# Kernel tuning notes

Measured on AMD Instinct MI355X. Metric: run time of the kernel, lower is better.

## Reference

```python
import jax, jax.numpy as jnp
import numpy as np
from jax import lax

B, S, D, NH, K = 4, 2048, 1024, 16, 3
EPS = 1e-6


def custom_layernorm(x, gamma, beta):
    # torch-style: std with ddof=1, eps added to std (not var)
    mean = jnp.mean(x, axis=-1, keepdims=True)
    var = jnp.sum((x - mean) ** 2, axis=-1, keepdims=True) / (x.shape[-1] - 1)
    std = jnp.sqrt(var)
    return gamma * ((x - mean) / (std + EPS)) + beta


def setup_inputs() -> dict:
    key = jax.random.key(0)
    ks = jax.random.split(key, 10)
    s = 1.0 / np.sqrt(D)
    return {
        "x": jax.random.normal(ks[0], (B, S, D), jnp.float32),
        "Wq": jax.random.normal(ks[1], (D, D), jnp.float32) * s,
        "bq": jax.random.normal(ks[2], (D,), jnp.float32) * 0.02,
        "Wk": jax.random.normal(ks[3], (D, D), jnp.float32) * s,
        "Wv": jax.random.normal(ks[4], (D, D), jnp.float32) * s,
        "bv": jax.random.normal(ks[5], (D,), jnp.float32) * 0.02,
        "conv_w": jax.random.normal(ks[6], (D, D // NH, K), jnp.float32) * (1.0 / np.sqrt((D // NH) * K)),
        "conv_b": jax.random.normal(ks[7], (D,), jnp.float32) * 0.02,
        "gamma": jnp.ones((D,), jnp.float32),
        "beta": jnp.zeros((D,), jnp.float32),
        "Wo": jax.random.normal(ks[8], (D, D), jnp.float32) * s,
        "bo": jax.random.normal(ks[9], (D,), jnp.float32) * 0.02,
    }


def reference(x, Wq, bq, Wk, Wv, bv, conv_w, conv_b, gamma, beta, Wo, bo):
    d = x.shape[-1]
    groups = d // conv_w.shape[1]
    pad = conv_w.shape[2] // 2

    q = x @ Wq + bq
    k = x @ Wk  # key has no bias
    v = x @ Wv + bv

    # grouped conv1d over sequence dim (NCW layout)
    xc = jnp.transpose(x, (0, 2, 1))  # [B, D, S]
    conv_out = lax.conv_general_dilated(
        xc, conv_w, window_strides=(1,), padding=[(pad, pad)],
        feature_group_count=groups,
        dimension_numbers=("NCH", "OIH", "NCH"),
    ) + conv_b[None, :, None]
    conv_out = jnp.transpose(conv_out, (0, 2, 1))  # [B, S, D]
    conv_out = custom_layernorm(conv_out, gamma, beta)  # dropout = identity (eval)

    scale = 1.0 / jnp.sqrt(jnp.asarray(d, x.dtype))
    scores = jnp.einsum("bqd,bkd->bqk", q, k) * scale  # [B, S, S]
    attn = jax.nn.softmax(scores, axis=-1)
    attention_out = jnp.einsum("bqk,bkd->bqd", attn, v)

    combined = custom_layernorm(conv_out + attention_out, gamma, beta)
    return combined @ Wo + bo + x
```

## Files before the change

### kernel.cpp

```cpp
#include <hip/hip_runtime.h>
#include <cstdint>


#define DEV __device__ __forceinline__

typedef unsigned short u16;
typedef __attribute__((ext_vector_type(8))) short bf16x8;
typedef __attribute__((ext_vector_type(4))) float f32x4;

static const int Sn = 2048, Dn = 1024;

DEV float bf2f(u16 u) { union { unsigned int i; float f; } w; w.i = ((unsigned int)u) << 16; return w.f; }
DEV u16 f2bf(float f) {
  union { float f; unsigned int i; } w; w.f = f;
  unsigned int x = w.i;
  return (u16)((x + 0x7FFFu + ((x >> 16) & 1u)) >> 16);
}

DEV void gload_lds16(const u16* gsrc, u16* lds_dst) {
  __builtin_amdgcn_global_load_lds(
      (const __attribute__((address_space(1))) void*)gsrc,
      (__attribute__((address_space(3))) void*)lds_dst,
      16, 0, 0);
}

DEV float block_allreduce_sum(float v, float* red, int tid) {
  #pragma unroll
  for (int o = 32; o > 0; o >>= 1) v += __shfl_down(v, o, 64);
  __syncthreads();
  if ((tid & 63) == 0) red[tid >> 6] = v;
  __syncthreads();
  return red[0] + red[1] + red[2] + red[3];
}

DEV float block_allreduce_max(float v, float* red, int tid) {
  #pragma unroll
  for (int o = 32; o > 0; o >>= 1) v = fmaxf(v, __shfl_down(v, o, 64));
  __syncthreads();
  if ((tid & 63) == 0) red[tid >> 6] = v;
  __syncthreads();
  return fmaxf(fmaxf(red[0], red[1]), fmaxf(red[2], red[3]));
}

__global__ __launch_bounds__(256)
void prep_all(const float* __restrict__ Wq, const float* __restrict__ Wk,
              const float* __restrict__ Wv, const float* __restrict__ Wo,
              u16* __restrict__ wT,
              const float* __restrict__ bq, const float* __restrict__ bv,
              float* __restrict__ qkvb, float* __restrict__ rowsum,
              const float* __restrict__ x, u16* __restrict__ xb) {
  __shared__ u16 sm[64][68];
  int blk = blockIdx.x;
  int tid = threadIdx.x;
  if (blk < 1024) {
    int w = blk >> 8, t = blk & 255;
    const float* src = (w == 0) ? Wq : (w == 1) ? Wk : (w == 2) ? Wv : Wo;
    u16* dst = wT + (size_t)w * 1048576u;
    int i0 = (t >> 4) << 6, j0 = (t & 15) << 6;
    int tx = tid & 15, r0 = tid >> 4;
    #pragma unroll
    for (int rr = r0; rr < 64; rr += 16) {
      float4 v = *(const float4*)&src[(long)(i0 + rr) * 1024 + j0 + tx * 4];
      sm[rr][tx*4+0] = f2bf(v.x); sm[rr][tx*4+1] = f2bf(v.y);
      sm[rr][tx*4+2] = f2bf(v.z); sm[rr][tx*4+3] = f2bf(v.w);
    }
    __syncthreads();
    #pragma unroll
    for (int cc = r0; cc < 64; cc += 16) {
      ushort4 o;
      o.x = sm[tx*4+0][cc]; o.y = sm[tx*4+1][cc];
      o.z = sm[tx*4+2][cc]; o.w = sm[tx*4+3][cc];
      *(ushort4*)&dst[(long)(j0 + cc) * 1024 + i0 + tx * 4] = o;
    }
  } else if (blk == 1024) {
    for (int j = tid; j < 3072; j += 256) {
      float v = 0.0f;
      if (j < 1024) v = bq[j];
      else if (j >= 2048) v = bv[j - 2048];
      qkvb[j] = v;
    }
    for (int j = tid; j < 8192; j += 256) rowsum[j] = 0.0f;
  } else {
    int i = (blk - 1025) * 1024 + tid * 4;
    float4 v = *(const float4*)&x[i];
    ushort4 o;
    o.x = f2bf(v.x); o.y = f2bf(v.y); o.z = f2bf(v.z); o.w = f2bf(v.w);
    *(ushort4*)&xb[i] = o;
  }
}

template<typename CT>
__global__ __launch_bounds__(256, 2)
void gemm_nt(const u16* __restrict__ A, const u16* __restrict__ A2, long Abs, int lda,
             const u16* __restrict__ B, long Bbs, int ldb,
             CT* __restrict__ C, CT* __restrict__ C2, long Cbs, int ldc,
             int zsplit, int K, float scale,
             const float* __restrict__ bias, int bias_bs,
             const float* __restrict__ res, long Rbs, int ldr,
             u16* __restrict__ vtout) {
  __shared__ u16 sA[2][128 * 32];
  __shared__ u16 sB[2][128 * 32];
  int tid = threadIdx.x;
  int lane = tid & 63, wv = tid >> 6;
  int quad = lane >> 4, lm = lane & 15;
  int wr = wv >> 1, wc = wv & 1;
  long m0 = (long)blockIdx.x * 128, n0 = (long)blockIdx.y * 128;
  int z = blockIdx.z;
  if (z >= zsplit) { A = A2 + (long)(z - zsplit) * Abs; C = C2 + (long)(z - zsplit) * Cbs; }
  else             { A = A  + (long)z * Abs;            C = C  + (long)z * Cbs; }
  B += (long)z * Bbs;
  if (res) res += (long)z * Rbs;

  f32x4 acc[4][4] = {};

  int srow = wv * 16 + (lane >> 2);
  int sch = (lane & 3) * 8;
  const u16* Ap = A + (m0 + srow) * (long)lda + sch;
  const u16* Bp = B + (n0 + srow) * (long)ldb + sch;
  const int lofs = wv * 16 * 32;

  for (int k0 = 0; k0 < K; k0 += 64) {
    #pragma unroll
    for (int h = 0; h < 2; h++) {
      int kh = k0 + h * 32;
      gload_lds16(Ap + kh, &sA[h][lofs]);
      gload_lds16(Ap + 64 * (long)lda + kh, &sA[h][lofs + 64 * 32]);
      gload_lds16(Bp + kh, &sB[h][lofs]);
      gload_lds16(Bp + 64 * (long)ldb + kh, &sB[h][lofs + 64 * 32]);
    }
    __syncthreads();
    #pragma unroll
    for (int h = 0; h < 2; h++) {
      bf16x8 af[4], bfr[4];
      #pragma unroll
      for (int mi = 0; mi < 4; mi++)
        af[mi] = *(const bf16x8*)&sA[h][(wr * 64 + mi * 16 + lm) * 32 + quad * 8];
      #pragma unroll
      for (int ni = 0; ni < 4; ni++)
        bfr[ni] = *(const bf16x8*)&sB[h][(wc * 64 + ni * 16 + lm) * 32 + quad * 8];
      #pragma unroll
      for (int mi = 0; mi < 4; mi++)
        #pragma unroll
        for (int ni = 0; ni < 4; ni++)
          acc[mi][ni] = __builtin_amdgcn_mfma_f32_16x16x32_bf16(af[mi], bfr[ni], acc[mi][ni], 0, 0, 0);
    }
    __syncthreads();
  }

  if (sizeof(CT) == 2 && vtout && z == 2) {
    int b = (int)(m0 >> 11);
    long s0 = (m0 & 2047) + wr * 64 + quad * 4;
    #pragma unroll
    for (int ni = 0; ni < 4; ni++) {
      int col = (int)n0 + wc * 64 + ni * 16 + lm;
      float bv = bias ? bias[(long)z * bias_bs + col] : 0.0f;
      u16* vrow = vtout + ((long)b * 1024 + col) * 2048;
      #pragma unroll
      for (int mi = 0; mi < 4; mi++) {
        ushort4 o;
        o.x = f2bf(acc[mi][ni][0] * scale + bv);
        o.y = f2bf(acc[mi][ni][1] * scale + bv);
        o.z = f2bf(acc[mi][ni][2] * scale + bv);
        o.w = f2bf(acc[mi][ni][3] * scale + bv);
        *(ushort4*)&vrow[s0 + mi * 16] = o;
      }
    }
  } else {
    #pragma unroll
    for (int mi = 0; mi < 4; mi++) {
      #pragma unroll
      for (int ni = 0; ni < 4; ni++) {
        int col = (int)n0 + wc * 64 + ni * 16 + lm;
        float bv = bias ? bias[(long)z * bias_bs + col] : 0.0f;
        #pragma unroll
        for (int r = 0; r < 4; r++) {
          long rowg = m0 + wr * 64 + mi * 16 + quad * 4 + r;
          float v = acc[mi][ni][r] * scale + bv;
          if (res) v += res[rowg * (long)ldr + col];
          if constexpr (sizeof(CT) == 2) C[rowg * (long)ldc + col] = f2bf(v);
          else                           C[rowg * (long)ldc + col] = v;
        }
      }
    }
  }
}

__global__ __launch_bounds__(256, 2)
void post_qkv(int ngemm,
              const u16* __restrict__ Qb, const u16* __restrict__ Kb,
              u16* __restrict__ Pd, u16* __restrict__ Pw,
              const u16* __restrict__ Vb, u16* __restrict__ vt,
              float* __restrict__ rowsum) {
  __shared__ u16 smem[2 * 2 * 128 * 32];
  int blk = blockIdx.x;
  int tid = threadIdx.x;
  if (blk < ngemm) {
    u16* sA0 = smem;
    u16* sB0 = smem + 2 * 128 * 32;
    int lane = tid & 63, wv = tid >> 6;
    int quad = lane >> 4, lm = lane & 15;
    int wr = wv >> 1, wc = wv & 1;
    int z = blk >> 8;
    long m0 = (long)(blk & 15) * 128, n0 = (long)((blk >> 4) & 15) * 128;
    const u16* A = Qb + (long)z * Sn * Dn;
    const u16* B = Kb + (long)z * Sn * Dn;
    u16* C = (z < 2) ? Pd + (long)z * Sn * Sn : Pw + (long)(z - 2) * Sn * Sn;

    f32x4 acc[4][4] = {};
    int srow = wv * 16 + (lane >> 2);
    int sch = (lane & 3) * 8;
    const u16* Ap = A + (m0 + srow) * 1024 + sch;
    const u16* Bp = B + (n0 + srow) * 1024 + sch;
    const int lofs = wv * 16 * 32;

    for (int k0 = 0; k0 < 1024; k0 += 64) {
      #pragma unroll
      for (int h = 0; h < 2; h++) {
        int kh = k0 + h * 32;
        gload_lds16(Ap + kh, &sA0[h * 128 * 32 + lofs]);
        gload_lds16(Ap + 64 * 1024 + kh, &sA0[h * 128 * 32 + lofs + 64 * 32]);
        gload_lds16(Bp + kh, &sB0[h * 128 * 32 + lofs]);
        gload_lds16(Bp + 64 * 1024 + kh, &sB0[h * 128 * 32 + lofs + 64 * 32]);
      }
      __syncthreads();
      #pragma unroll
      for (int h = 0; h < 2; h++) {
        bf16x8 af[4], bfr[4];
        #pragma unroll
        for (int mi = 0; mi < 4; mi++)
          af[mi] = *(const bf16x8*)&sA0[h * 128 * 32 + (wr * 64 + mi * 16 + lm) * 32 + quad * 8];
        #pragma unroll
        for (int ni = 0; ni < 4; ni++)
          bfr[ni] = *(const bf16x8*)&sB0[h * 128 * 32 + (wc * 64 + ni * 16 + lm) * 32 + quad * 8];
        #pragma unroll
        for (int mi = 0; mi < 4; mi++)
          #pragma unroll
          for (int ni = 0; ni < 4; ni++)
            acc[mi][ni] = __builtin_amdgcn_mfma_f32_16x16x32_bf16(af[mi], bfr[ni], acc[mi][ni], 0, 0, 0);
      }
      __syncthreads();
    }
    float psum[4][4];
    #pragma unroll
    for (int mi = 0; mi < 4; mi++)
      #pragma unroll
      for (int r = 0; r < 4; r++) psum[mi][r] = 0.0f;
    #pragma unroll
    for (int mi = 0; mi < 4; mi++) {
      #pragma unroll
      for (int ni = 0; ni < 4; ni++) {
        int col = (int)n0 + wc * 64 + ni * 16 + lm;
        #pragma unroll
        for (int r = 0; r < 4; r++) {
          long rowg = m0 + wr * 64 + mi * 16 + quad * 4 + r;
          float e = __expf(acc[mi][ni][r] * 0.03125f);
          psum[mi][r] += e;
          C[rowg * 2048 + col] = f2bf(e);
        }
      }
    }
    #pragma unroll
    for (int mi = 0; mi < 4; mi++)
      #pragma unroll
      for (int r = 0; r < 4; r++) {
        float v = psum[mi][r];
        v += __shfl_xor(v, 1, 64);
        v += __shfl_xor(v, 2, 64);
        v += __shfl_xor(v, 4, 64);
        v += __shfl_xor(v, 8, 64);
        psum[mi][r] = v;
      }
    if (lm == 0) {
      #pragma unroll
      for (int mi = 0; mi < 4; mi++)
        #pragma unroll
        for (int r = 0; r < 4; r++) {
          long rowg = m0 + wr * 64 + mi * 16 + quad * 4 + r;
          unsafeAtomicAdd(&rowsum[(long)z * 2048 + rowg], psum[mi][r]);
        }
    }
  } else {
    u16 (*sm)[68] = (u16(*)[68])smem;
    int t = blk - ngemm;
    int b = t >> 9, r = t & 511;
    int j0 = (r & 15) << 6, i0 = ((r >> 4) & 31) << 6;
    const u16* s = Vb + (long)b * Sn * Dn;
    u16* d = vt + (long)b * Dn * Sn;
    int tx = tid & 15, r0 = tid >> 4;
    #pragma unroll
    for (int rr = r0; rr < 64; rr += 16) {
      ushort4 v = *(const ushort4*)&s[(long)(i0 + rr) * 1024 + j0 + tx * 4];
      sm[rr][tx*4+0] = v.x; sm[rr][tx*4+1] = v.y; sm[rr][tx*4+2] = v.z; sm[rr][tx*4+3] = v.w;
    }
    __syncthreads();
    #pragma unroll
    for (int cc = r0; cc < 64; cc += 16) {
      ushort4 o;
      o.x = sm[tx*4+0][cc]; o.y = sm[tx*4+1][cc];
      o.z = sm[tx*4+2][cc]; o.w = sm[tx*4+3][cc];
      *(ushort4*)&d[(long)(j0 + cc) * 2048 + i0 + tx * 4] = o;
    }
  }
}

__global__ __launch_bounds__(256)
void smax_conv(u16* __restrict__ pa, u16* __restrict__ pb, int rowsplit, int nsm,
               const float* __restrict__ x, const float* __restrict__ cw,
               const float* __restrict__ cb, u16* __restrict__ convo) {
  __shared__ u16 smem[22160];
  __shared__ float red[4];
  int blk = blockIdx.x;
  int tid = threadIdx.x;
  if (blk < nsm) {
    long row = blk;
    u16* p = (row < rowsplit) ? pa + row * 2048 : pb + (row - rowsplit) * 2048;
    ushort4 a = *(const ushort4*)&p[tid * 8];
    ushort4 b = *(const ushort4*)&p[tid * 8 + 4];
    float f0 = bf2f(a.x), f1 = bf2f(a.y), f2 = bf2f(a.z), f3 = bf2f(a.w);
    float f4 = bf2f(b.x), f5 = bf2f(b.y), f6 = bf2f(b.z), f7 = bf2f(b.w);
    float m = fmaxf(fmaxf(fmaxf(f0, f1), fmaxf(f2, f3)),
                    fmaxf(fmaxf(f4, f5), fmaxf(f6, f7)));
    m = block_allreduce_max(m, red, tid);
    float e0 = __expf(f0 - m), e1 = __expf(f1 - m), e2 = __expf(f2 - m), e3 = __expf(f3 - m);
    float e4 = __expf(f4 - m), e5 = __expf(f5 - m), e6 = __expf(f6 - m), e7 = __expf(f7 - m);
    float s = block_allreduce_sum(e0 + e1 + e2 + e3 + e4 + e5 + e6 + e7, red, tid);
    float inv = 1.0f / s;
    ushort4 o1, o2;
    o1.x = f2bf(e0 * inv); o1.y = f2bf(e1 * inv); o1.z = f2bf(e2 * inv); o1.w = f2bf(e3 * inv);
    o2.x = f2bf(e4 * inv); o2.y = f2bf(e5 * inv); o2.z = f2bf(e6 * inv); o2.w = f2bf(e7 * inv);
    *(ushort4*)&p[tid * 8] = o1;
    *(ushort4*)&p[tid * 8 + 4] = o2;
  } else {
    u16 (*sx)[72] = (u16(*)[72])smem;
    u16 (*sw)[200] = (u16(*)[200])(smem + 9360);
    int r = blk - nsm;
    int s0 = (r & 15) * 128;
    int g = (r >> 4) & 15;
    int b = r >> 8;
    int lane = tid & 63, wv = tid >> 6;
    int quad = lane >> 4, lm = lane & 15;
    for (int idx = tid; idx < 64 * 192; idx += 256) {
      int oc = idx / 192, k = idx - oc * 192;
      int t2 = k >> 6, i = k & 63;
      sw[oc][k] = f2bf(cw[((long)(g * 64 + oc)) * 192 + i * 3 + t2]);
    }
    for (int idx = tid; idx < 130 * 16; idx += 256) {
      int rr = idx >> 4, c4 = (idx & 15) * 4;
      int s = s0 - 1 + rr;
      ushort4 v;
      if (s >= 0 && s < Sn) {
        float4 f = *(const float4*)&x[((long)b * Sn + s) * Dn + g * 64 + c4];
        v.x = f2bf(f.x); v.y = f2bf(f.y); v.z = f2bf(f.z); v.w = f2bf(f.w);
      } else { v.x = 0; v.y = 0; v.z = 0; v.w = 0; }
      *(ushort4*)&sx[rr][c4] = v;
    }
    __syncthreads();
    f32x4 acc[2][4] = {};
    #pragma unroll
    for (int ks = 0; ks < 6; ks++) {
      int t2 = ks >> 1;
      int i0 = (ks & 1) * 32 + quad * 8;
      bf16x8 a0 = *(const bf16x8*)&sx[wv * 32 + lm + t2][i0];
      bf16x8 a1 = *(const bf16x8*)&sx[wv * 32 + 16 + lm + t2][i0];
      #pragma unroll
      for (int nf = 0; nf < 4; nf++) {
        bf16x8 bf = *(const bf16x8*)&sw[nf * 16 + lm][ks * 32 + quad * 8];
        acc[0][nf] = __builtin_amdgcn_mfma_f32_16x16x32_bf16(a0, bf, acc[0][nf], 0, 0, 0);
        acc[1][nf] = __builtin_amdgcn_mfma_f32_16x16x32_bf16(a1, bf, acc[1][nf], 0, 0, 0);
      }
    }
    #pragma unroll
    for (int mi = 0; mi < 2; mi++) {
      #pragma unroll
      for (int nf = 0; nf < 4; nf++) {
        int col = g * 64 + nf * 16 + lm;
        float bias = cb[col];
        #pragma unroll
        for (int rr = 0; rr < 4; rr++) {
          int row = wv * 32 + mi * 16 + quad * 4 + rr;
          convo[((long)b * Sn + s0 + row) * Dn + col] = f2bf(acc[mi][nf][rr] + bias);
        }
      }
    }
  }
}

__global__ __launch_bounds__(256, 2)
void pv_conv(int npv,
             const u16* __restrict__ Pd, const u16* __restrict__ Pw,
             const u16* __restrict__ vt, u16* __restrict__ attn,
             const float* __restrict__ rowsum,
             const float* __restrict__ x, const float* __restrict__ cw,
             const float* __restrict__ cb, u16* __restrict__ convo) {
  __shared__ u16 smem[22160];
  int blk = blockIdx.x;
  int tid = threadIdx.x;
  if (blk < npv) {
    u16* sA0 = smem;
    u16* sB0 = smem + 2 * 128 * 32;
    int lane = tid & 63, wv = tid >> 6;
    int quad = lane >> 4, lm = lane & 15;
    int wr = wv >> 1, wc = wv & 1;
    int z = blk >> 7;
    long m0 = (long)(blk & 15) * 128, n0 = (long)((blk >> 4) & 7) * 128;
    const u16* A = (z < 2) ? Pd + (long)z * Sn * Sn : Pw + (long)(z - 2) * Sn * Sn;
    const u16* B = vt + (long)z * Dn * Sn;
    u16* C = attn + (long)z * Sn * Dn;

    f32x4 acc[4][4] = {};
    int srow = wv * 16 + (lane >> 2);
    int sch = (lane & 3) * 8;
    const u16* Ap = A + (m0 + srow) * 2048 + sch;
    const u16* Bp = B + (n0 + srow) * 2048 + sch;
    const int lofs = wv * 16 * 32;

    for (int k0 = 0; k0 < 2048; k0 += 64) {
      #pragma unroll
      for (int h = 0; h < 2; h++) {
        int kh = k0 + h * 32;
        gload_lds16(Ap + kh, &sA0[h * 128 * 32 + lofs]);
        gload_lds16(Ap + 64 * 2048 + kh, &sA0[h * 128 * 32 + lofs + 64 * 32]);
        gload_lds16(Bp + kh, &sB0[h * 128 * 32 + lofs]);
        gload_lds16(Bp + 64 * 2048 + kh, &sB0[h * 128 * 32 + lofs + 64 * 32]);
      }
      __syncthreads();
      #pragma unroll
      for (int h = 0; h < 2; h++) {
        bf16x8 af[4], bfr[4];
        #pragma unroll
        for (int mi = 0; mi < 4; mi++)
          af[mi] = *(const bf16x8*)&sA0[h * 128 * 32 + (wr * 64 + mi * 16 + lm) * 32 + quad * 8];
        #pragma unroll
        for (int ni = 0; ni < 4; ni++)
          bfr[ni] = *(const bf16x8*)&sB0[h * 128 * 32 + (wc * 64 + ni * 16 + lm) * 32 + quad * 8];
        #pragma unroll
        for (int mi = 0; mi < 4; mi++)
          #pragma unroll
          for (int ni = 0; ni < 4; ni++)
            acc[mi][ni] = __builtin_amdgcn_mfma_f32_16x16x32_bf16(af[mi], bfr[ni], acc[mi][ni], 0, 0, 0);
      }
      __syncthreads();
    }
    float inv[4][4];
    #pragma unroll
    for (int mi = 0; mi < 4; mi++)
      #pragma unroll
      for (int r = 0; r < 4; r++) {
        long rowg = m0 + wr * 64 + mi * 16 + quad * 4 + r;
        inv[mi][r] = 1.0f / rowsum[(long)z * 2048 + rowg];
      }
    #pragma unroll
    for (int mi = 0; mi < 4; mi++) {
      #pragma unroll
      for (int ni = 0; ni < 4; ni++) {
        int col = (int)n0 + wc * 64 + ni * 16 + lm;
        #pragma unroll
        for (int r = 0; r < 4; r++) {
          long rowg = m0 + wr * 64 + mi * 16 + quad * 4 + r;
          C[rowg * 1024 + col] = f2bf(acc[mi][ni][r] * inv[mi][r]);
        }
      }
    }
  } else {
    u16 (*sx)[72] = (u16(*)[72])smem;
    u16 (*sw)[200] = (u16(*)[200])(smem + 9360);
    int r = blk - npv;
    int s0 = (r & 15) * 128;
    int g = (r >> 4) & 15;
    int b = r >> 8;
    int lane = tid & 63, wv = tid >> 6;
    int quad = lane >> 4, lm = lane & 15;
    for (int idx = tid; idx < 64 * 192; idx += 256) {
      int oc = idx / 192, k = idx - oc * 192;
      int t2 = k >> 6, i = k & 63;
      sw[oc][k] = f2bf(cw[((long)(g * 64 + oc)) * 192 + i * 3 + t2]);
    }
    for (int idx = tid; idx < 130 * 16; idx += 256) {
      int rr = idx >> 4, c4 = (idx & 15) * 4;
      int s = s0 - 1 + rr;
      ushort4 v;
      if (s >= 0 && s < Sn) {
        float4 f = *(const float4*)&x[((long)b * Sn + s) * Dn + g * 64 + c4];
        v.x = f2bf(f.x); v.y = f2bf(f.y); v.z = f2bf(f.z); v.w = f2bf(f.w);
      } else { v.x = 0; v.y = 0; v.z = 0; v.w = 0; }
      *(ushort4*)&sx[rr][c4] = v;
    }
    __syncthreads();
    f32x4 acc[2][4] = {};
    #pragma unroll
    for (int ks = 0; ks < 6; ks++) {
      int t2 = ks >> 1;
      int i0 = (ks & 1) * 32 + quad * 8;
      bf16x8 a0 = *(const bf16x8*)&sx[wv * 32 + lm + t2][i0];
      bf16x8 a1 = *(const bf16x8*)&sx[wv * 32 + 16 + lm + t2][i0];
      #pragma unroll
      for (int nf = 0; nf < 4; nf++) {
        bf16x8 bf = *(const bf16x8*)&sw[nf * 16 + lm][ks * 32 + quad * 8];
        acc[0][nf] = __builtin_amdgcn_mfma_f32_16x16x32_bf16(a0, bf, acc[0][nf], 0, 0, 0);
        acc[1][nf] = __builtin_amdgcn_mfma_f32_16x16x32_bf16(a1, bf, acc[1][nf], 0, 0, 0);
      }
    }
    #pragma unroll
    for (int mi = 0; mi < 2; mi++) {
      #pragma unroll
      for (int nf = 0; nf < 4; nf++) {
        int col = g * 64 + nf * 16 + lm;
        float bias = cb[col];
        #pragma unroll
        for (int rr = 0; rr < 4; rr++) {
          int row = wv * 32 + mi * 16 + quad * 4 + rr;
          convo[((long)b * Sn + s0 + row) * Dn + col] = f2bf(acc[mi][nf][rr] + bias);
        }
      }
    }
  }
}

__global__ __launch_bounds__(256)
void ln2_kernel(const u16* __restrict__ conv, const u16* __restrict__ attn,
                const float* __restrict__ gamma, const float* __restrict__ beta,
                u16* __restrict__ out) {
  __shared__ float red[4];
  int tid = threadIdx.x;
  long base = (long)blockIdx.x * Dn + tid * 4;
  ushort4 cv = *(const ushort4*)&conv[base];
  float c0 = bf2f(cv.x), c1 = bf2f(cv.y), c2 = bf2f(cv.z), c3 = bf2f(cv.w);
  float4 gv = *(const float4*)&gamma[tid * 4];
  float4 bev = *(const float4*)&beta[tid * 4];
  float s1 = block_allreduce_sum(c0 + c1 + c2 + c3, red, tid);
  float mean1 = s1 * (1.0f / 1024.0f);
  float d0 = c0 - mean1, d1 = c1 - mean1, d2 = c2 - mean1, d3 = c3 - mean1;
  float sq1 = block_allreduce_sum(d0 * d0 + d1 * d1 + d2 * d2 + d3 * d3, red, tid);
  float inv1 = 1.0f / (sqrtf(sq1 * (1.0f / 1023.0f)) + 1e-6f);
  ushort4 av = *(const ushort4*)&attn[base];
  float v0 = gv.x * d0 * inv1 + bev.x + bf2f(av.x);
  float v1 = gv.y * d1 * inv1 + bev.y + bf2f(av.y);
  float v2 = gv.z * d2 * inv1 + bev.z + bf2f(av.z);
  float v3 = gv.w * d3 * inv1 + bev.w + bf2f(av.w);
  float s2 = block_allreduce_sum(v0 + v1 + v2 + v3, red, tid);
  float mean2 = s2 * (1.0f / 1024.0f);
  float e0 = v0 - mean2, e1 = v1 - mean2, e2 = v2 - mean2, e3 = v3 - mean2;
  float sq2 = block_allreduce_sum(e0 * e0 + e1 * e1 + e2 * e2 + e3 * e3, red, tid);
  float inv2 = 1.0f / (sqrtf(sq2 * (1.0f / 1023.0f)) + 1e-6f);
  ushort4 o;
  o.x = f2bf(gv.x * e0 * inv2 + bev.x);
  o.y = f2bf(gv.y * e1 * inv2 + bev.y);
  o.z = f2bf(gv.z * e2 * inv2 + bev.z);
  o.w = f2bf(gv.w * e3 * inv2 + bev.w);
  *(ushort4*)&out[base] = o;
}

static const size_t OFF_WT    = 0;
static const size_t OFF_QKVB  = 8ull << 20;
static const size_t OFF_RSUM  = (8ull << 20) + (16 << 10);
static const size_t OFF_Q     = 9ull << 20;
static const size_t OFF_K     = 25ull << 20;
static const size_t OFF_V     = 41ull << 20;
static const size_t OFF_PW    = 57ull << 20;

extern "C" void kernel_launch(void* const* d_in, const int* in_sizes, int n_in,
                              void* d_out, int out_size, void* d_ws, size_t ws_size,
                              hipStream_t stream) {
  const float* x     = (const float*)d_in[0];
  const float* Wq    = (const float*)d_in[1];
  const float* bq    = (const float*)d_in[2];
  const float* Wk    = (const float*)d_in[3];
  const float* Wv    = (const float*)d_in[4];
  const float* bv    = (const float*)d_in[5];
  const float* cw    = (const float*)d_in[6];
  const float* cb    = (const float*)d_in[7];
  const float* gamma = (const float*)d_in[8];
  const float* beta  = (const float*)d_in[9];
  const float* Wo    = (const float*)d_in[10];
  const float* bo    = (const float*)d_in[11];
  float* out = (float*)d_out;
  char* ws = (char*)d_ws;

  u16*   wT    = (u16*)(ws + OFF_WT);
  float* qkvb  = (float*)(ws + OFF_QKVB);
  float* rsum  = (float*)(ws + OFF_RSUM);
  u16*   Qb    = (u16*)(ws + OFF_Q);
  u16*   Kb    = (u16*)(ws + OFF_K);
  u16*   Vb    = (u16*)(ws + OFF_V);
  u16*   Pw    = (u16*)(ws + OFF_PW);
  u16*   xb    = (u16*)d_out;
  u16*   Pd    = (u16*)d_out;
  u16*   vt    = (u16*)d_out + 8388608;
  u16*   conv  = Vb;
  u16*   attn  = Qb;
  u16*   combined = Kb;
  const long PBS = (long)Sn * Sn;

  dim3 tb(256);

  prep_all<<<dim3(9217), tb, 0, stream>>>(Wq, Wk, Wv, Wo, wT, bq, bv, qkvb,
                                          rsum, x, xb);

  if (ws_size >= (73ull << 20)) {
    gemm_nt<u16><<<dim3(64, 8, 3), tb, 0, stream>>>(
        xb, nullptr, 0, 1024, wT, 1048576, 1024, Qb, (u16*)nullptr, 8388608, 1024,
        99, 1024, 1.0f, qkvb, 1024, nullptr, 0, 0, vt);
    post_qkv<<<dim3(1024), tb, 0, stream>>>(1024, Qb, Kb, Pd, Pw, Vb, vt, rsum);
    pv_conv<<<dim3(512 + 1024), tb, 0, stream>>>(512, Pd, Pw, vt, attn, rsum,
                                                 x, cw, cb, conv);
    ln2_kernel<<<dim3(8192), tb, 0, stream>>>(conv, attn, gamma, beta, combined);
  } else {
    gemm_nt<u16><<<dim3(64, 8, 3), tb, 0, stream>>>(
        xb, nullptr, 0, 1024, wT, 1048576, 1024, Qb, (u16*)nullptr, 8388608, 1024,
        99, 1024, 1.0f, qkvb, 1024, nullptr, 0, 0, nullptr);
    post_qkv<<<dim3(2048), tb, 0, stream>>>(0, Qb, Kb, Pd, Pw, Vb, vt, rsum);
    for (int c = 0; c < 2; c++) {
      long off = (long)c * 2 * Sn * Dn;
      gemm_nt<u16><<<dim3(16, 16, 2), tb, 0, stream>>>(
          Qb + off, nullptr, (long)Sn * Dn, 1024, Kb + off, (long)Sn * Dn, 1024,
          Pd, (u16*)nullptr, PBS, 2048,
          99, 1024, 0.03125f, nullptr, 0, nullptr, 0, 0, nullptr);
      smax_conv<<<dim3(4096 + (c == 0 ? 1024 : 0)), tb, 0, stream>>>(
          Pd, Pd, 4096, 4096, x, cw, cb, conv);
      gemm_nt<u16><<<dim3(16, 8, 2), tb, 0, stream>>>(
          Pd, nullptr, PBS, 2048, vt + off, (long)Dn * Sn, 2048,
          attn + off, (u16*)nullptr, (long)Sn * Dn, 1024,
          99, 2048, 1.0f, nullptr, 0, nullptr, 0, 0, nullptr);
    }
    ln2_kernel<<<dim3(8192), tb, 0, stream>>>(conv, attn, gamma, beta, combined);
  }

  gemm_nt<float><<<dim3(64, 8, 1), tb, 0, stream>>>(
      combined, nullptr, 0, 1024, wT + 3u * 1048576u, 0, 1024,
      out, (float*)nullptr, 0, 1024,
      99, 1024, 1.0f, bo, 0, x, 0, 1024, nullptr);
}
```

Before: 329.4 us.

## Reassociate QK^T through precomputed Wk·Wq^T to drop the K projection

```diff
diff --git a/kernel.cpp b/kernel.cpp
--- a/kernel.cpp
+++ b/kernel.cpp
@@ -48,7 +48,9 @@
               u16* __restrict__ wT,
               const float* __restrict__ bq, const float* __restrict__ bv,
               float* __restrict__ qkvb, float* __restrict__ rowsum,
-              const float* __restrict__ x, u16* __restrict__ xb) {
+              const float* __restrict__ x, u16* __restrict__ xb,
+              u16* __restrict__ wqo, u16* __restrict__ wko,
+              float* __restrict__ wbout) {
   __shared__ u16 sm[64][68];
   int blk = blockIdx.x;
   int tid = threadIdx.x;
@@ -80,12 +82,40 @@
       qkvb[j] = v;
     }
     for (int j = tid; j < 8192; j += 256) rowsum[j] = 0.0f;
-  } else {
+  } else if (blk < 9217) {
     int i = (blk - 1025) * 1024 + tid * 4;
     float4 v = *(const float4*)&x[i];
     ushort4 o;
     o.x = f2bf(v.x); o.y = f2bf(v.y); o.z = f2bf(v.z); o.w = f2bf(v.w);
     *(ushort4*)&xb[i] = o;
+  } else if (blk < 11265) {
+    int idx = blk - 9217;
+    int w = idx >> 10;
+    long i = (long)(idx & 1023) * 1024 + tid * 4;
+    const float* src = w ? Wk : Wq;
+    u16* dst = w ? wko : wqo;
+    float4 v = *(const float4*)&src[i];
+    ushort4 o;
+    o.x = f2bf(v.x); o.y = f2bf(v.y); o.z = f2bf(v.z); o.w = f2bf(v.w);
+    *(ushort4*)&dst[i] = o;
+  } else {
+    int t = blk - 11265;
+    int lane = tid & 63, wv2 = tid >> 6;
+    for (int rr = 0; rr < 16; rr++) {
+      int e = t * 64 + wv2 * 16 + rr;
+      const float* wr = Wk + (long)e * 1024 + lane * 16;
+      const float* br = bq + lane * 16;
+      float s = 0.0f;
+      #pragma unroll
+      for (int j = 0; j < 16; j += 4) {
+        float4 a4 = *(const float4*)&wr[j];
+        float4 b4 = *(const float4*)&br[j];
+        s += a4.x * b4.x + a4.y * b4.y + a4.z * b4.z + a4.w * b4.w;
+      }
+      #pragma unroll
+      for (int o = 32; o > 0; o >>= 1) s += __shfl_down(s, o, 64);
+      if (lane == 0) wbout[e] = s;
+    }
   }
 }
 
@@ -186,11 +216,116 @@
 }
 
 __global__ __launch_bounds__(256, 2)
+void vg_kv(const u16* __restrict__ xb, const u16* __restrict__ wvT,
+           const u16* __restrict__ wqo, const u16* __restrict__ wko,
+           const float* __restrict__ bv,
+           u16* __restrict__ vt, u16* __restrict__ G,
+           const float* __restrict__ wb, float* __restrict__ kv) {
+  __shared__ u16 sA[2][128 * 32];
+  __shared__ u16 sB[2][128 * 32];
+  int blk = blockIdx.x;
+  int tid = threadIdx.x;
+  if (blk < 576) {
+    bool isV = blk < 512;
+    long m0, n0;
+    const u16 *A, *B;
+    if (isV) { m0 = (long)(blk & 63) * 128; n0 = (long)(blk >> 6) * 128; A = xb; B = wvT; }
+    else { int t = blk - 512; m0 = (long)(t & 7) * 128; n0 = (long)(t >> 3) * 128; A = wko; B = wqo; }
+    int lane = tid & 63, wv = tid >> 6;
+    int quad = lane >> 4, lm = lane & 15;
+    int wr = wv >> 1, wc = wv & 1;
+    f32x4 acc[4][4] = {};
+    int srow = wv * 16 + (lane >> 2);
+    int sch = (lane & 3) * 8;
+    const u16* Ap = A + (m0 + srow) * 1024 + sch;
+    const u16* Bp = B + (n0 + srow) * 1024 + sch;
+    const int lofs = wv * 16 * 32;
+    for (int k0 = 0; k0 < 1024; k0 += 64) {
+      #pragma unroll
+      for (int h = 0; h < 2; h++) {
+        int kh = k0 + h * 32;
+        gload_lds16(Ap + kh, &sA[h][lofs]);
+        gload_lds16(Ap + 64 * 1024 + kh, &sA[h][lofs + 64 * 32]);
+        gload_lds16(Bp + kh, &sB[h][lofs]);
+        gload_lds16(Bp + 64 * 1024 + kh, &sB[h][lofs + 64 * 32]);
+      }
+      __syncthreads();
+      #pragma unroll
+      for (int h = 0; h < 2; h++) {
+        bf16x8 af[4], bfr[4];
+        #pragma unroll
+        for (int mi = 0; mi < 4; mi++)
+          af[mi] = *(const bf16x8*)&sA[h][(wr * 64 + mi * 16 + lm) * 32 + quad * 8];
+        #pragma unroll
+        for (int ni = 0; ni < 4; ni++)
+          bfr[ni] = *(const bf16x8*)&sB[h][(wc * 64 + ni * 16 + lm) * 32 + quad * 8];
+        #pragma unroll
+        for (int mi = 0; mi < 4; mi++)
+          #pragma unroll
+          for (int ni = 0; ni < 4; ni++)
+            acc[mi][ni] = __builtin_amdgcn_mfma_f32_16x16x32_bf16(af[mi], bfr[ni], acc[mi][ni], 0, 0, 0);
+      }
+      __syncthreads();
+    }
+    if (isV) {
+      int b = (int)(m0 >> 11);
+      long s0 = (m0 & 2047) + wr * 64 + quad * 4;
+      #pragma unroll
+      for (int ni = 0; ni < 4; ni++) {
+        int col = (int)n0 + wc * 64 + ni * 16 + lm;
+        float bvv = bv[col];
+        u16* vrow = vt + ((long)b * 1024 + col) * 2048;
+        #pragma unroll
+        for (int mi = 0; mi < 4; mi++) {
+          ushort4 o;
+          o.x = f2bf(acc[mi][ni][0] + bvv);
+          o.y = f2bf(acc[mi][ni][1] + bvv);
+          o.z = f2bf(acc[mi][ni][2] + bvv);
+          o.w = f2bf(acc[mi][ni][3] + bvv);
+          *(ushort4*)&vrow[s0 + mi * 16] = o;
+        }
+      }
+    } else {
+      #pragma unroll
+      for (int mi = 0; mi < 4; mi++) {
+        #pragma unroll
+        for (int ni = 0; ni < 4; ni++) {
+          int col = (int)n0 + wc * 64 + ni * 16 + lm;
+          #pragma unroll
+          for (int r = 0; r < 4; r++) {
+            long rowg = m0 + wr * 64 + mi * 16 + quad * 4 + r;
+            G[rowg * 1024 + col] = f2bf(acc[mi][ni][r]);
+          }
+        }
+      }
+    }
+  } else {
+    int t = blk - 576;
+    int lane = tid & 63, wv2 = tid >> 6;
+    for (int rr = 0; rr < 32; rr++) {
+      long row = (long)t * 128 + wv2 * 32 + rr;
+      const u16* xr = xb + row * 1024 + lane * 16;
+      const float* wr = wb + lane * 16;
+      float s = 0.0f;
+      #pragma unroll
+      for (int j = 0; j < 16; j += 4) {
+        ushort4 v = *(const ushort4*)&xr[j];
+        float4 w4 = *(const float4*)&wr[j];
+        s += bf2f(v.x) * w4.x + bf2f(v.y) * w4.y + bf2f(v.z) * w4.z + bf2f(v.w) * w4.w;
+      }
+      #pragma unroll
+      for (int o = 32; o > 0; o >>= 1) s += __shfl_down(s, o, 64);
+      if (lane == 0) kv[row] = s;
+    }
+  }
+}
+
+__global__ __launch_bounds__(256, 2)
 void post_qkv(int ngemm,
-              const u16* __restrict__ Qb, const u16* __restrict__ Kb,
+              const u16* __restrict__ Qb, const u16* __restrict__ Bx,
               u16* __restrict__ Pd, u16* __restrict__ Pw,
               const u16* __restrict__ Vb, u16* __restrict__ vt,
-              float* __restrict__ rowsum) {
+              float* __restrict__ rowsum, const float* __restrict__ kv) {
   __shared__ u16 smem[2 * 2 * 128 * 32];
   int blk = blockIdx.x;
   int tid = threadIdx.x;
@@ -203,7 +338,7 @@
     int z = blk >> 8;
     long m0 = (long)(blk & 15) * 128, n0 = (long)((blk >> 4) & 15) * 128;
     const u16* A = Qb + (long)z * Sn * Dn;
-    const u16* B = Kb + (long)z * Sn * Dn;
+    const u16* B = Bx + (long)z * Sn * Dn;
     u16* C = (z < 2) ? Pd + (long)z * Sn * Sn : Pw + (long)(z - 2) * Sn * Sn;
 
     f32x4 acc[4][4] = {};
@@ -240,6 +375,12 @@
       }
       __syncthreads();
     }
+    float kvv[4];
+    #pragma unroll
+    for (int ni = 0; ni < 4; ni++) {
+      int col = (int)n0 + wc * 64 + ni * 16 + lm;
+      kvv[ni] = kv ? kv[(long)z * 2048 + col] : 0.0f;
+    }
     float psum[4][4];
     #pragma unroll
     for (int mi = 0; mi < 4; mi++)
@@ -253,7 +394,7 @@
         #pragma unroll
         for (int r = 0; r < 4; r++) {
           long rowg = m0 + wr * 64 + mi * 16 + quad * 4 + r;
-          float e = __expf(acc[mi][ni][r] * 0.03125f);
+          float e = __expf((acc[mi][ni][r] + kvv[ni]) * 0.03125f);
           psum[mi][r] += e;
           C[rowg * 2048 + col] = f2bf(e);
         }
@@ -552,7 +693,9 @@
 
 static const size_t OFF_WT    = 0;
 static const size_t OFF_QKVB  = 8ull << 20;
+static const size_t OFF_WB    = (8ull << 20) + (12 << 10);
 static const size_t OFF_RSUM  = (8ull << 20) + (16 << 10);
+static const size_t OFF_KV    = (8ull << 20) + (48 << 10);
 static const size_t OFF_Q     = 9ull << 20;
 static const size_t OFF_K     = 25ull << 20;
 static const size_t OFF_V     = 41ull << 20;
@@ -578,13 +721,16 @@
 
   u16*   wT    = (u16*)(ws + OFF_WT);
   float* qkvb  = (float*)(ws + OFF_QKVB);
+  float* wb    = (float*)(ws + OFF_WB);
   float* rsum  = (float*)(ws + OFF_RSUM);
+  float* kv    = (float*)(ws + OFF_KV);
   u16*   Qb    = (u16*)(ws + OFF_Q);
   u16*   Kb    = (u16*)(ws + OFF_K);
   u16*   Vb    = (u16*)(ws + OFF_V);
   u16*   Pw    = (u16*)(ws + OFF_PW);
+  u16*   wqo   = Pw;
+  u16*   wko   = Pw + 1048576;
   u16*   xb    = (u16*)d_out;
-  u16*   Pd    = (u16*)d_out;
   u16*   vt    = (u16*)d_out + 8388608;
   u16*   conv  = Vb;
   u16*   attn  = Qb;
@@ -593,22 +739,28 @@
 
   dim3 tb(256);
 
-  prep_all<<<dim3(9217), tb, 0, stream>>>(Wq, Wk, Wv, Wo, wT, bq, bv, qkvb,
-                                          rsum, x, xb);
-
   if (ws_size >= (73ull << 20)) {
-    gemm_nt<u16><<<dim3(64, 8, 3), tb, 0, stream>>>(
-        xb, nullptr, 0, 1024, wT, 1048576, 1024, Qb, (u16*)nullptr, 8388608, 1024,
-        99, 1024, 1.0f, qkvb, 1024, nullptr, 0, 0, vt);
-    post_qkv<<<dim3(1024), tb, 0, stream>>>(1024, Qb, Kb, Pd, Pw, Vb, vt, rsum);
-    pv_conv<<<dim3(512 + 1024), tb, 0, stream>>>(512, Pd, Pw, vt, attn, rsum,
+    prep_all<<<dim3(11281), tb, 0, stream>>>(Wq, Wk, Wv, Wo, wT, bq, bv, qkvb,
+                                             rsum, x, xb, wqo, wko, wb);
+    vg_kv<<<dim3(640), tb, 0, stream>>>(xb, wT + 2u * 1048576u, wqo, wko,
+                                        qkvb + 2048, vt, wT, wb, kv);
+    gemm_nt<u16><<<dim3(64, 8, 1), tb, 0, stream>>>(
+        xb, nullptr, 0, 1024, wT, 0, 1024, Qb, (u16*)nullptr, 0, 1024,
+        99, 1024, 1.0f, nullptr, 0, nullptr, 0, 0, nullptr);
+    post_qkv<<<dim3(1024), tb, 0, stream>>>(1024, Qb, xb, Kb, Pw, Vb, vt,
+                                            rsum, kv);
+    pv_conv<<<dim3(512 + 1024), tb, 0, stream>>>(512, Kb, Pw, vt, attn, rsum,
                                                  x, cw, cb, conv);
     ln2_kernel<<<dim3(8192), tb, 0, stream>>>(conv, attn, gamma, beta, combined);
   } else {
+    prep_all<<<dim3(11281), tb, 0, stream>>>(Wq, Wk, Wv, Wo, wT, bq, bv, qkvb,
+                                             rsum, x, xb, wqo, wko, wb);
+    u16* Pd = (u16*)d_out;
     gemm_nt<u16><<<dim3(64, 8, 3), tb, 0, stream>>>(
         xb, nullptr, 0, 1024, wT, 1048576, 1024, Qb, (u16*)nullptr, 8388608, 1024,
         99, 1024, 1.0f, qkvb, 1024, nullptr, 0, 0, nullptr);
-    post_qkv<<<dim3(2048), tb, 0, stream>>>(0, Qb, Kb, Pd, Pw, Vb, vt, rsum);
+    post_qkv<<<dim3(2048), tb, 0, stream>>>(0, Qb, Kb, Pd, Pw, Vb, vt, rsum,
+                                            nullptr);
     for (int c = 0; c < 2; c++) {
       long off = (long)c * 2 * Sn * Dn;
       gemm_nt<u16><<<dim3(16, 16, 2), tb, 0, stream>>>(
```

After: 344.6 us. 4.6% more time.
